# Performance work log

Hardware: AMD Instinct MI355X
Metric: run time of the kernel (lower is better)

## Reference

```python
import jax, jax.numpy as jnp
import numpy as np

T, B, D, H, O = 512, 64, 512, 1024, 512

def _xavier(key, shape):
    fan_out, fan_in = shape
    limit = np.sqrt(6.0 / (fan_in + fan_out))
    return jax.random.uniform(key, shape, jnp.float32, -limit, limit)

def setup_inputs() -> dict:
    key = jax.random.key(0)
    ks = jax.random.split(key, 10)
    x = jax.random.normal(ks[0], (T, B, D), jnp.float32)
    # Gate order: i, f, o, c (stacked along first axis for a fused 4H projection;
    # math identical to 8 separate Linears in the torch module, biases init to 0
    # but we randomize them slightly for a non-trivial reference).
    Wx = jnp.concatenate([_xavier(ks[1 + g], (H, D)) for g in range(4)], axis=0)  # [4H, D]
    Wh = jnp.concatenate([_xavier(ks[5 + g], (H, H)) for g in range(4)], axis=0)  # [4H, H]
    bx = jnp.zeros((4 * H,), jnp.float32)
    bh = jnp.zeros((4 * H,), jnp.float32)
    Why = _xavier(ks[9], (O, H))
    bhy = jnp.zeros((O,), jnp.float32)
    return {"x": x, "Wx": Wx, "bx": bx, "Wh": Wh, "bh": bh, "Why": Why, "bhy": bhy}

def reference(x, Wx, bx, Wh, bh, Why, bhy):
    Hd = Wh.shape[1]
    Bd = x.shape[1]
    # Precompute all input-path projections in one batched GEMM: [T, B, 4H]
    xp = jnp.einsum('tbd,gd->tbg', x, Wx) + bx + bh

    def step(carry, xp_t):
        h, c = carry
        gates = xp_t + h @ Wh.T  # [B, 4H]
        i_t = jax.nn.sigmoid(gates[:, 0 * Hd:1 * Hd])
        f_t = jax.nn.sigmoid(gates[:, 1 * Hd:2 * Hd])
        o_t = jax.nn.sigmoid(gates[:, 2 * Hd:3 * Hd])
        c_tilde = jnp.tanh(gates[:, 3 * Hd:4 * Hd])
        c = f_t * c + i_t * c_tilde
        h = o_t * jnp.tanh(c)
        return (h, c), None

    h0 = jnp.zeros((Bd, Hd), x.dtype)
    c0 = jnp.zeros((Bd, Hd), x.dtype)
    (h, c), _ = jax.lax.scan(step, (h0, c0), xp)
    return h @ Why.T + bhy  # [B, O]
```

## Files before the change

kernel.cpp:

```cpp
#include <hip/hip_runtime.h>
#include <hip/hip_bf16.h>
#include <math.h>

constexpr int T = 512;
constexpr int B = 64;
constexpr int D = 512;
constexpr int H = 1024;
constexpr int O = 512;
constexpr int GROUPS = 2;
constexpr int BG   = B / GROUPS;
constexpr int GBLK = 128;
constexpr int COLS = 32;
constexpr int KCH  = (D + H) / 8;

typedef __attribute__((ext_vector_type(8))) __bf16 bf16x8;
typedef __attribute__((ext_vector_type(4))) float  floatx4;

struct GBar {
    unsigned grp[8][32];
    unsigned root; unsigned p0[31];
    unsigned gflag[8][32];
};

__global__ __launch_bounds__(256) void convert_w(
    const float* __restrict__ Wx, const float* __restrict__ Wh,
    __bf16* __restrict__ Wc)
{
    const int id = blockIdx.x * 256 + threadIdx.x;
    if (id >= GBLK * KCH * COLS) return;
    const int nl     = id & 31;
    const int kchunk = (id >> 5) % KCH;
    const int strip  = id / (KCH * COLS);
    const int n = strip * COLS + nl;
    const int j = n >> 2, g = n & 3;
    const int k0 = kchunk * 8;
    const float* src = (k0 < D) ? &Wx[(size_t)(g * H + j) * D + k0]
                                : &Wh[(size_t)(g * H + j) * H + (k0 - D)];
    const float4 a = *(const float4*)src;
    const float4 b = *(const float4*)(src + 4);
    __bf16 t8[8] = {(__bf16)a.x,(__bf16)a.y,(__bf16)a.z,(__bf16)a.w,
                    (__bf16)b.x,(__bf16)b.y,(__bf16)b.z,(__bf16)b.w};
    *(uint4*)&Wc[(size_t)id * 8] = *(uint4*)t8;
}

__global__ __launch_bounds__(256) void make_bias(
    const float* __restrict__ bx, const float* __restrict__ bh,
    float* __restrict__ bias)
{
    const int n = blockIdx.x * 256 + threadIdx.x;
    if (n < 4 * H) {
        const int j = n >> 2, g = n & 3;
        bias[n] = bx[g * H + j] + bh[g * H + j];
    }
}

__global__ __launch_bounds__(128, 1) void lstm_persistent(
    const float* __restrict__ x,
    const __bf16* __restrict__ Wc,
    const float* __restrict__ bias,
    __bf16* __restrict__ hbufs,
    float* __restrict__ hfin,
    GBar* bars)
{
    __shared__ __attribute__((aligned(16))) __bf16 wlds[KCH * COLS * 8];
    __shared__ __attribute__((aligned(16))) float  G[32][COLS + 4];

    const int tid   = threadIdx.x;
    const int wid   = tid >> 6;
    const int lane  = tid & 63;
    const int cm    = lane & 15;
    const int q     = lane >> 4;
    const int group = blockIdx.x >> 7;
    const int gb    = blockIdx.x & 127;
    const int n0    = gb * COLS;
    GBar* bar = bars + group;
    __bf16* hb0 = hbufs + (size_t)group * 2 * BG * H;
    __bf16* hb1 = hb0 + BG * H;

    {
        const uint4* wsrc = (const uint4*)(Wc + (size_t)gb * KCH * COLS * 8);
        uint4* wdst = (uint4*)wlds;
        for (int i = tid; i < KCH * COLS; i += 128) wdst[i] = wsrc[i];
    }
    const int eb = tid >> 2;
    const int p  = tid & 3;
    const int jbase = (n0 >> 2) + p * 2;
    const float4 bias0 = *(const float4*)&bias[n0 + p * 8];
    const float4 bias1 = *(const float4*)&bias[n0 + p * 8 + 4];
    float c0 = 0.f, c1 = 0.f;
    __syncthreads();

    const int grow = group * BG + wid * 16 + cm;
    const float* xrow = x + (size_t)grow * D + q * 8;
    const int    hoff = (wid * 16 + cm) * H + q * 8;
    const __bf16* wl  = wlds + (q * 32 + cm) * 8;

    floatx4 acc[2][2];
    float4  xcur[16][2];

    auto loadx = [&](int tt) {
        const float* xr = xrow + (size_t)tt * (B * D);
        #pragma unroll
        for (int s = 0; s < 16; ++s) {
            xcur[s][0] = *(const float4*)(xr + s * 32);
            xcur[s][1] = *(const float4*)(xr + s * 32 + 4);
        }
    };
    auto xmfma = [&]() {
        acc[0][0] = (floatx4){0,0,0,0}; acc[0][1] = (floatx4){0,0,0,0};
        acc[1][0] = (floatx4){0,0,0,0}; acc[1][1] = (floatx4){0,0,0,0};
        #pragma unroll
        for (int s = 0; s < 16; ++s) {
            const float4 a0 = xcur[s][0], a1 = xcur[s][1];
            const bf16x8 af = {(__bf16)a0.x,(__bf16)a0.y,(__bf16)a0.z,(__bf16)a0.w,
                               (__bf16)a1.x,(__bf16)a1.y,(__bf16)a1.z,(__bf16)a1.w};
            const bf16x8 b0 = *(const bf16x8*)(wl + s * 1024);
            const bf16x8 b1 = *(const bf16x8*)(wl + s * 1024 + 128);
            acc[0][s & 1] = __builtin_amdgcn_mfma_f32_16x16x32_bf16(af, b0, acc[0][s & 1], 0, 0, 0);
            acc[1][s & 1] = __builtin_amdgcn_mfma_f32_16x16x32_bf16(af, b1, acc[1][s & 1], 0, 0, 0);
        }
    };

    loadx(0);
    xmfma();

    const int sub = gb >> 4;

    for (int t = 0; t < T; ++t) {
        const __bf16* hcur = (t & 1) ? hb1 : hb0;
        __bf16*       hnxt = (t & 1) ? hb0 : hb1;

        if (t > 0) {
            if (tid == 0) {
                while (__hip_atomic_load(&bar->gflag[sub][0], __ATOMIC_RELAXED,
                                         __HIP_MEMORY_SCOPE_AGENT) < (unsigned)t)
                    __builtin_amdgcn_s_sleep(1);
            }
            __syncthreads();
        }

        {
            const __bf16* hbase = hcur + hoff;
            uint4 hv[32];
            asm volatile(
                "global_load_dwordx4 %0, %32, off sc0 sc1\n\t"
                "global_load_dwordx4 %1, %32, off offset:64 sc0 sc1\n\t"
                "global_load_dwordx4 %2, %32, off offset:128 sc0 sc1\n\t"
                "global_load_dwordx4 %3, %32, off offset:192 sc0 sc1\n\t"
                "global_load_dwordx4 %4, %32, off offset:256 sc0 sc1\n\t"
                "global_load_dwordx4 %5, %32, off offset:320 sc0 sc1\n\t"
                "global_load_dwordx4 %6, %32, off offset:384 sc0 sc1\n\t"
                "global_load_dwordx4 %7, %32, off offset:448 sc0 sc1\n\t"
                "global_load_dwordx4 %8, %32, off offset:512 sc0 sc1\n\t"
                "global_load_dwordx4 %9, %32, off offset:576 sc0 sc1\n\t"
                "global_load_dwordx4 %10, %32, off offset:640 sc0 sc1\n\t"
                "global_load_dwordx4 %11, %32, off offset:704 sc0 sc1\n\t"
                "global_load_dwordx4 %12, %32, off offset:768 sc0 sc1\n\t"
                "global_load_dwordx4 %13, %32, off offset:832 sc0 sc1\n\t"
                "global_load_dwordx4 %14, %32, off offset:896 sc0 sc1\n\t"
                "global_load_dwordx4 %15, %32, off offset:960 sc0 sc1\n\t"
                "global_load_dwordx4 %16, %32, off offset:1024 sc0 sc1\n\t"
                "global_load_dwordx4 %17, %32, off offset:1088 sc0 sc1\n\t"
                "global_load_dwordx4 %18, %32, off offset:1152 sc0 sc1\n\t"
                "global_load_dwordx4 %19, %32, off offset:1216 sc0 sc1\n\t"
                "global_load_dwordx4 %20, %32, off offset:1280 sc0 sc1\n\t"
                "global_load_dwordx4 %21, %32, off offset:1344 sc0 sc1\n\t"
                "global_load_dwordx4 %22, %32, off offset:1408 sc0 sc1\n\t"
                "global_load_dwordx4 %23, %32, off offset:1472 sc0 sc1\n\t"
                "global_load_dwordx4 %24, %32, off offset:1536 sc0 sc1\n\t"
                "global_load_dwordx4 %25, %32, off offset:1600 sc0 sc1\n\t"
                "global_load_dwordx4 %26, %32, off offset:1664 sc0 sc1\n\t"
                "global_load_dwordx4 %27, %32, off offset:1728 sc0 sc1\n\t"
                "global_load_dwordx4 %28, %32, off offset:1792 sc0 sc1\n\t"
                "global_load_dwordx4 %29, %32, off offset:1856 sc0 sc1\n\t"
                "global_load_dwordx4 %30, %32, off offset:1920 sc0 sc1\n\t"
                "global_load_dwordx4 %31, %32, off offset:1984 sc0 sc1\n\t"
                "s_waitcnt vmcnt(0)"
                : "=&v"(hv[0]),  "=&v"(hv[1]),  "=&v"(hv[2]),  "=&v"(hv[3]),
                  "=&v"(hv[4]),  "=&v"(hv[5]),  "=&v"(hv[6]),  "=&v"(hv[7]),
                  "=&v"(hv[8]),  "=&v"(hv[9]),  "=&v"(hv[10]), "=&v"(hv[11]),
                  "=&v"(hv[12]), "=&v"(hv[13]), "=&v"(hv[14]), "=&v"(hv[15]),
                  "=&v"(hv[16]), "=&v"(hv[17]), "=&v"(hv[18]), "=&v"(hv[19]),
                  "=&v"(hv[20]), "=&v"(hv[21]), "=&v"(hv[22]), "=&v"(hv[23]),
                  "=&v"(hv[24]), "=&v"(hv[25]), "=&v"(hv[26]), "=&v"(hv[27]),
                  "=&v"(hv[28]), "=&v"(hv[29]), "=&v"(hv[30]), "=&v"(hv[31])
                : "v"(hbase)
                : "memory");
            #pragma unroll
            for (int sg = 0; sg < 32; ++sg) {
                union { uint4 u; bf16x8 v; } hf; hf.u = hv[sg];
                const bf16x8 b0 = *(const bf16x8*)(wl + 16384 + sg * 1024);
                const bf16x8 b1 = *(const bf16x8*)(wl + 16384 + sg * 1024 + 128);
                acc[0][sg & 1] = __builtin_amdgcn_mfma_f32_16x16x32_bf16(hf.v, b0, acc[0][sg & 1], 0, 0, 0);
                acc[1][sg & 1] = __builtin_amdgcn_mfma_f32_16x16x32_bf16(hf.v, b1, acc[1][sg & 1], 0, 0, 0);
            }
        }
        const floatx4 av0 = acc[0][0] + acc[0][1];
        const floatx4 av1 = acc[1][0] + acc[1][1];

        #pragma unroll
        for (int r = 0; r < 4; ++r) {
            G[wid * 16 + q * 4 + r][cm]      = av0[r];
            G[wid * 16 + q * 4 + r][16 + cm] = av1[r];
        }

        if (t + 1 < T) loadx(t + 1);

        __syncthreads();

        const float4 g0 = *(const float4*)&G[eb][p * 8];
        const float4 g1 = *(const float4*)&G[eb][p * 8 + 4];
        const float i0 = 1.f / (1.f + expf(-(g0.x + bias0.x)));
        const float f0 = 1.f / (1.f + expf(-(g0.y + bias0.y)));
        const float o0 = 1.f / (1.f + expf(-(g0.z + bias0.z)));
        const float t0 = tanhf(g0.w + bias0.w);
        const float i1 = 1.f / (1.f + expf(-(g1.x + bias1.x)));
        const float f1 = 1.f / (1.f + expf(-(g1.y + bias1.y)));
        const float o1 = 1.f / (1.f + expf(-(g1.z + bias1.z)));
        const float t1 = tanhf(g1.w + bias1.w);
        c0 = f0 * c0 + i0 * t0;
        c1 = f1 * c1 + i1 * t1;
        const float hv0 = o0 * tanhf(c0);
        const float hv1 = o1 * tanhf(c1);
        const int hi = eb * H + jbase;
        union { __bf16 h2[2]; unsigned u; } hp;
        hp.h2[0] = (__bf16)hv0; hp.h2[1] = (__bf16)hv1;
        __hip_atomic_store((unsigned*)&hnxt[hi], hp.u, __ATOMIC_RELAXED,
                           __HIP_MEMORY_SCOPE_AGENT);
        if (t == T - 1) {
            const int gr = group * BG + eb;
            hfin[gr * H + jbase] = hv0; hfin[gr * H + jbase + 1] = hv1;
        }

        __syncthreads();

        if (tid == 0) {
            const unsigned old = __hip_atomic_fetch_add(&bar->grp[sub][0], 1u,
                                    __ATOMIC_RELAXED, __HIP_MEMORY_SCOPE_AGENT);
            if (old == 16u * (unsigned)(t + 1) - 1u) {
                const unsigned r = __hip_atomic_fetch_add(&bar->root, 1u,
                                    __ATOMIC_RELAXED, __HIP_MEMORY_SCOPE_AGENT);
                if (r == 8u * (unsigned)(t + 1) - 1u) {
                    #pragma unroll
                    for (int k = 0; k < 8; ++k)
                        __hip_atomic_store(&bar->gflag[k][0], (unsigned)(t + 1),
                                           __ATOMIC_RELAXED, __HIP_MEMORY_SCOPE_AGENT);
                }
            }
        }
        if (t + 1 < T) xmfma();
    }
}

__global__ __launch_bounds__(256) void out_gemm(
    const float* __restrict__ h, const float* __restrict__ Why,
    const float* __restrict__ bhy, float* __restrict__ out)
{
    const int idx = blockIdx.x * 256 + threadIdx.x;
    if (idx >= B * O) return;
    const int b = idx / O;
    const int o = idx % O;
    const float4* hv = (const float4*)&h[(size_t)b * H];
    const float4* wv = (const float4*)&Why[(size_t)o * H];
    float s = 0.f;
    #pragma unroll 4
    for (int k = 0; k < H / 4; ++k) {
        const float4 a = hv[k];
        const float4 w = wv[k];
        s += a.x * w.x + a.y * w.y + a.z * w.z + a.w * w.w;
    }
    out[idx] = s + bhy[o];
}

extern "C" void kernel_launch(void* const* d_in, const int* in_sizes, int n_in,
                              void* d_out, int out_size, void* d_ws, size_t ws_size,
                              hipStream_t stream) {
    const float* x   = (const float*)d_in[0];
    const float* Wx  = (const float*)d_in[1];
    const float* bx  = (const float*)d_in[2];
    const float* Wh  = (const float*)d_in[3];
    const float* bh  = (const float*)d_in[4];
    const float* Why = (const float*)d_in[5];
    const float* bhy = (const float*)d_in[6];
    float* out = (float*)d_out;

    char* ws = (char*)d_ws;
    __bf16* Wc    = (__bf16*)ws;
    float*  bias  = (float*)(ws + 12582912);
    __bf16* hbufs = (__bf16*)(ws + 12599296);
    GBar*   bars  = (GBar*)  (ws + 12861440);
    float*  hfin  = (float*)ws;

    (void)hipMemsetAsync(ws + 12599296, 0, 262144 + 8192, stream);
    convert_w<<<3072, 256, 0, stream>>>(Wx, Wh, Wc);
    make_bias<<<16, 256, 0, stream>>>(bx, bh, bias);

    lstm_persistent<<<GROUPS * GBLK, 128, 0, stream>>>(x, Wc, bias, hbufs,
                                                       hfin, bars);

    out_gemm<<<(B * O + 255) / 256, 256, 0, stream>>>(hfin, Why, bhy, out);
}
```

Before: 3.503 ms.

## Replace LDS gate transpose with quad shuffles and use flag-array grid barrier

Removes the shared-memory G staging buffer and one __syncthreads by transposing MFMA accumulator fragments within lane quads via shuffles, so each lane computes the gate nonlinearities directly from registers and writes two separate bf16 h values. The hierarchical atomic-counter barrier is replaced by per-block arrival flags polled by block 0's first wavefront with a ballot, which then publishes the group flags. All threads now spin on the group flag instead of a single thread plus syncthreads. Risks include more narrow 16-bit atomic stores, a serial polling bottleneck in block 0 that delays its own next step, and relaxed-ordering visibility concerns.

```diff
diff --git a/kernel.cpp b/kernel.cpp
--- a/kernel.cpp
+++ b/kernel.cpp
@@ -17,8 +17,7 @@
 typedef __attribute__((ext_vector_type(4))) float  floatx4;
 
 struct GBar {
-    unsigned grp[8][32];
-    unsigned root; unsigned p0[31];
+    unsigned arr[GBLK][32];
     unsigned gflag[8][32];
 };
 
@@ -63,7 +62,6 @@
     GBar* bars)
 {
     __shared__ __attribute__((aligned(16))) __bf16 wlds[KCH * COLS * 8];
-    __shared__ __attribute__((aligned(16))) float  G[32][COLS + 4];
 
     const int tid   = threadIdx.x;
     const int wid   = tid >> 6;
@@ -82,11 +80,11 @@
         uint4* wdst = (uint4*)wlds;
         for (int i = tid; i < KCH * COLS; i += 128) wdst[i] = wsrc[i];
     }
-    const int eb = tid >> 2;
-    const int p  = tid & 3;
-    const int jbase = (n0 >> 2) + p * 2;
-    const float4 bias0 = *(const float4*)&bias[n0 + p * 8];
-    const float4 bias1 = *(const float4*)&bias[n0 + p * 8 + 4];
+    const int p4 = cm & 3;
+    const int jl = cm >> 2;
+    const int row_l = wid * 16 + q * 4 + p4;
+    const float4 bias0q = *(const float4*)&bias[n0 + jl * 4];
+    const float4 bias1q = *(const float4*)&bias[n0 + 16 + jl * 4];
     float c0 = 0.f, c1 = 0.f;
     __syncthreads();
 
@@ -121,6 +119,15 @@
         }
     };
 
+    auto quadT = [&](float v[4]) {
+        float w0 = __shfl_xor(v[1], 1), w1 = __shfl_xor(v[0], 1);
+        float w2 = __shfl_xor(v[3], 1), w3 = __shfl_xor(v[2], 1);
+        if (p4 & 1) { v[0] = w0; v[2] = w2; } else { v[1] = w1; v[3] = w3; }
+        w0 = __shfl_xor(v[2], 2); w1 = __shfl_xor(v[3], 2);
+        w2 = __shfl_xor(v[0], 2); w3 = __shfl_xor(v[1], 2);
+        if (p4 & 2) { v[0] = w0; v[1] = w1; } else { v[2] = w2; v[3] = w3; }
+    };
+
     loadx(0);
     xmfma();
 
@@ -131,12 +138,9 @@
         __bf16*       hnxt = (t & 1) ? hb0 : hb1;
 
         if (t > 0) {
-            if (tid == 0) {
-                while (__hip_atomic_load(&bar->gflag[sub][0], __ATOMIC_RELAXED,
-                                         __HIP_MEMORY_SCOPE_AGENT) < (unsigned)t)
-                    __builtin_amdgcn_s_sleep(1);
-            }
-            __syncthreads();
+            while (__hip_atomic_load(&bar->gflag[sub][0], __ATOMIC_RELAXED,
+                                     __HIP_MEMORY_SCOPE_AGENT) < (unsigned)t)
+                __builtin_amdgcn_s_sleep(1);
         }
 
         {
@@ -198,57 +202,60 @@
         const floatx4 av0 = acc[0][0] + acc[0][1];
         const floatx4 av1 = acc[1][0] + acc[1][1];
 
-        #pragma unroll
-        for (int r = 0; r < 4; ++r) {
-            G[wid * 16 + q * 4 + r][cm]      = av0[r];
-            G[wid * 16 + q * 4 + r][16 + cm] = av1[r];
-        }
+        float g0v[4] = {av0.x, av0.y, av0.z, av0.w};
+        float g1v[4] = {av1.x, av1.y, av1.z, av1.w};
+        quadT(g0v);
+        quadT(g1v);
 
         if (t + 1 < T) loadx(t + 1);
 
-        __syncthreads();
-
-        const float4 g0 = *(const float4*)&G[eb][p * 8];
-        const float4 g1 = *(const float4*)&G[eb][p * 8 + 4];
-        const float i0 = 1.f / (1.f + expf(-(g0.x + bias0.x)));
-        const float f0 = 1.f / (1.f + expf(-(g0.y + bias0.y)));
-        const float o0 = 1.f / (1.f + expf(-(g0.z + bias0.z)));
-        const float t0 = tanhf(g0.w + bias0.w);
-        const float i1 = 1.f / (1.f + expf(-(g1.x + bias1.x)));
-        const float f1 = 1.f / (1.f + expf(-(g1.y + bias1.y)));
-        const float o1 = 1.f / (1.f + expf(-(g1.z + bias1.z)));
-        const float t1 = tanhf(g1.w + bias1.w);
+        const float i0 = 1.f / (1.f + expf(-(g0v[0] + bias0q.x)));
+        const float f0 = 1.f / (1.f + expf(-(g0v[1] + bias0q.y)));
+        const float o0 = 1.f / (1.f + expf(-(g0v[2] + bias0q.z)));
+        const float t0 = tanhf(g0v[3] + bias0q.w);
+        const float i1 = 1.f / (1.f + expf(-(g1v[0] + bias1q.x)));
+        const float f1 = 1.f / (1.f + expf(-(g1v[1] + bias1q.y)));
+        const float o1 = 1.f / (1.f + expf(-(g1v[2] + bias1q.z)));
+        const float t1 = tanhf(g1v[3] + bias1q.w);
         c0 = f0 * c0 + i0 * t0;
         c1 = f1 * c1 + i1 * t1;
         const float hv0 = o0 * tanhf(c0);
         const float hv1 = o1 * tanhf(c1);
-        const int hi = eb * H + jbase;
-        union { __bf16 h2[2]; unsigned u; } hp;
-        hp.h2[0] = (__bf16)hv0; hp.h2[1] = (__bf16)hv1;
-        __hip_atomic_store((unsigned*)&hnxt[hi], hp.u, __ATOMIC_RELAXED,
+        const int j0 = gb * 8 + jl;
+        const int hi = row_l * H + j0;
+        union { __bf16 b; unsigned short u; } s0, s1;
+        s0.b = (__bf16)hv0; s1.b = (__bf16)hv1;
+        __hip_atomic_store((unsigned short*)&hnxt[hi], s0.u, __ATOMIC_RELAXED,
+                           __HIP_MEMORY_SCOPE_AGENT);
+        __hip_atomic_store((unsigned short*)&hnxt[hi + 4], s1.u, __ATOMIC_RELAXED,
                            __HIP_MEMORY_SCOPE_AGENT);
         if (t == T - 1) {
-            const int gr = group * BG + eb;
-            hfin[gr * H + jbase] = hv0; hfin[gr * H + jbase + 1] = hv1;
+            const int gr = group * BG + row_l;
+            hfin[gr * H + j0]     = hv0;
+            hfin[gr * H + j0 + 4] = hv1;
         }
 
         __syncthreads();
 
-        if (tid == 0) {
-            const unsigned old = __hip_atomic_fetch_add(&bar->grp[sub][0], 1u,
-                                    __ATOMIC_RELAXED, __HIP_MEMORY_SCOPE_AGENT);
-            if (old == 16u * (unsigned)(t + 1) - 1u) {
-                const unsigned r = __hip_atomic_fetch_add(&bar->root, 1u,
-                                    __ATOMIC_RELAXED, __HIP_MEMORY_SCOPE_AGENT);
-                if (r == 8u * (unsigned)(t + 1) - 1u) {
-                    #pragma unroll
-                    for (int k = 0; k < 8; ++k)
-                        __hip_atomic_store(&bar->gflag[k][0], (unsigned)(t + 1),
-                                           __ATOMIC_RELAXED, __HIP_MEMORY_SCOPE_AGENT);
-                }
+        if (tid == 0)
+            __hip_atomic_store(&bar->arr[gb][0], (unsigned)(t + 1),
+                               __ATOMIC_RELAXED, __HIP_MEMORY_SCOPE_AGENT);
+
+        if (t + 1 < T) xmfma();
+
+        if (gb == 0 && tid < 64) {
+            const unsigned want = (unsigned)(t + 1);
+            for (;;) {
+                const unsigned a = __hip_atomic_load(&bar->arr[2 * tid][0],
+                                        __ATOMIC_RELAXED, __HIP_MEMORY_SCOPE_AGENT);
+                const unsigned b = __hip_atomic_load(&bar->arr[2 * tid + 1][0],
+                                        __ATOMIC_RELAXED, __HIP_MEMORY_SCOPE_AGENT);
+                if (__ballot((a >= want) && (b >= want)) == ~0ull) break;
             }
-        }
-        if (t + 1 < T) xmfma();
+            if (tid < 8)
+                __hip_atomic_store(&bar->gflag[tid][0], want,
+                                   __ATOMIC_RELAXED, __HIP_MEMORY_SCOPE_AGENT);
+        }
     }
 }
 
@@ -291,7 +298,7 @@
     GBar*   bars  = (GBar*)  (ws + 12861440);
     float*  hfin  = (float*)ws;
 
-    (void)hipMemsetAsync(ws + 12599296, 0, 262144 + 8192, stream);
+    (void)hipMemsetAsync(ws + 12599296, 0, 262144 + 2 * sizeof(GBar), stream);
     convert_w<<<3072, 256, 0, stream>>>(Wx, Wh, Wc);
     make_bias<<<16, 256, 0, stream>>>(bx, bh, bias);
 
```

After: 3.473 ms. No clear change (-0.8%).
